# Kernel optimization log

Measured on AMD Instinct MI355X. Metric: run time of the kernel, lower is better.

Reference implementation:

```python
import jax, jax.numpy as jnp
import numpy as np

B, N_OBJ, N_REL = 32, 100, 512
D_OBJ, D_CTX, D_HID = 1024, 1024, 1024


def setup_inputs() -> dict:
    key = jax.random.key(0)
    k1, k2, k3, k4, k5 = jax.random.split(key, 5)
    object_branch_output = jax.random.normal(k1, (B * N_OBJ, D_OBJ), dtype=jnp.float32)
    context_branch_output = jax.random.normal(k2, (B, D_CTX), dtype=jnp.float32)
    num_obj = jnp.full((B,), N_OBJ, dtype=jnp.int32)
    num_rels = jnp.full((B,), N_REL, dtype=jnp.int32)
    obj_pairs = jax.random.randint(k3, (B, N_REL, 2), 0, N_OBJ, dtype=jnp.int32)
    W1 = jax.random.normal(k4, (D_OBJ + D_CTX, D_HID), dtype=jnp.float32) * (1.0 / np.sqrt(D_OBJ + D_CTX))
    b1 = jnp.zeros((D_HID,), dtype=jnp.float32)
    W2 = jax.random.normal(k5, (D_HID, D_HID), dtype=jnp.float32) * (1.0 / np.sqrt(D_HID))
    b2 = jnp.zeros((D_HID,), dtype=jnp.float32)
    return {
        "object_branch_output": object_branch_output,
        "context_branch_output": context_branch_output,
        "num_obj": num_obj,
        "num_rels": num_rels,
        "obj_pairs": obj_pairs,
        "W1": W1, "b1": b1, "W2": W2, "b2": b2,
    }


def reference(object_branch_output, context_branch_output, num_obj, num_rels,
              obj_pairs, W1, b1, W2, b2):
    # --- prepare_f_oo_vis_input, fully vectorized ---
    # per-batch object index offsets: sum(num_obj[:b])  (exclusive cumsum)
    obj_offsets = jnp.cumsum(num_obj) - num_obj                       # [B]
    global_pairs = obj_pairs + obj_offsets[:, None, None]             # [B, R, 2]
    # gather both endpoints of every pair and mean-aggregate
    pair_feats = object_branch_output[global_pairs]                   # [B, R, 2, D_obj]
    obj_vec = pair_feats.mean(axis=2)                                 # [B, R, D_obj]
    # broadcast per-batch context vector to every relation, then concat
    ctx = jnp.broadcast_to(context_branch_output[:, None, :],
                           obj_vec.shape[:2] + (context_branch_output.shape[-1],))
    input_f_oo_vis = jnp.concatenate([obj_vec, ctx], axis=-1)         # [B, R, D_obj+D_ctx]
    x = input_f_oo_vis.reshape(-1, input_f_oo_vis.shape[-1])          # [tot_rels, D_obj+D_ctx]
    # --- f_oo_vis MLP: (Linear -> ReLU) per layer pair ---
    h = jax.nn.relu(x @ W1 + b1)
    f_oo_vis_output = jax.nn.relu(h @ W2 + b2)
    return object_branch_output, f_oo_vis_output
```

## Files before the change

kernel.cpp:

```cpp
#include <hip/hip_runtime.h>
#include <hip/hip_bf16.h>

#define BB   32
#define NREL 512
#define DD   1024
#define MTOT (BB * NREL)
#define OBJ_ROWS (BB * 100)

typedef __attribute__((ext_vector_type(8))) short bf16x8;
typedef __attribute__((ext_vector_type(4))) float f32x4;

__device__ __forceinline__ unsigned short f2bf(float f) {
    union { float f; unsigned u; } v; v.f = f;
    unsigned r = v.u + 0x7fff + ((v.u >> 16) & 1);
    return (unsigned short)(r >> 16);
}

__device__ __forceinline__ float bf2f(unsigned short s) {
    union { unsigned u; float f; } v; v.u = (unsigned)s << 16;
    return v.f;
}

__device__ __forceinline__ void gld16(const void* g, void* l) {
    __builtin_amdgcn_global_load_lds(
        (const __attribute__((address_space(1))) unsigned int*)g,
        (__attribute__((address_space(3))) unsigned int*)l,
        16, 0, 0);
}

__device__ __forceinline__ void barfence() {
    asm volatile("" ::: "memory");
    __builtin_amdgcn_s_barrier();
    asm volatile("" ::: "memory");
}

__global__ void __launch_bounds__(256) prep_kernel(
    const float* __restrict__ obj, const float* __restrict__ ctx,
    const float* __restrict__ W1, const float* __restrict__ W2,
    unsigned short* __restrict__ W1t, unsigned short* __restrict__ W2t,
    float* __restrict__ part, unsigned short* __restrict__ obj_bf,
    float* __restrict__ out_obj) {
    __shared__ float smem[32 * 33];
    int bid = blockIdx.x;
    int tid = threadIdx.x;

    if (bid < 1024) {
        int slice = bid & 3, chunk = (bid >> 2) & 7, b = bid >> 5;
        int nl = tid & 127, kh = tid >> 7;
        int n = chunk * 128 + nl;
        int kbase = slice * 256 + kh * 128;
        const float* c = ctx + (size_t)b * DD + kbase;
        const float* w = W1 + (size_t)(DD + kbase) * DD + n;
        float a0 = 0.f, a1 = 0.f, a2 = 0.f, a3 = 0.f;
#pragma unroll 8
        for (int k = 0; k < 128; k += 4) {
            a0 = fmaf(c[k + 0], w[(size_t)(k + 0) * DD], a0);
            a1 = fmaf(c[k + 1], w[(size_t)(k + 1) * DD], a1);
            a2 = fmaf(c[k + 2], w[(size_t)(k + 2) * DD], a2);
            a3 = fmaf(c[k + 3], w[(size_t)(k + 3) * DD], a3);
        }
        smem[kh * 128 + nl] = (a0 + a1) + (a2 + a3);
        __syncthreads();
        if (kh == 0)
            part[(((size_t)slice * BB + b) << 10) + n] = smem[nl] + smem[128 + nl];
    } else if (bid < 3072) {
        const float* W = (bid < 2048) ? W1 : W2;
        unsigned short* Wt = (bid < 2048) ? W1t : W2t;
        int t = (bid - 1024) & 1023;
        int k0 = (t >> 5) * 32, n0 = (t & 31) * 32;
        int tr = tid >> 5, tc = tid & 31;
#pragma unroll
        for (int i = 0; i < 4; i++)
            smem[(tr + i * 8) * 33 + tc] = W[(size_t)(k0 + tr + i * 8) * DD + n0 + tc];
        __syncthreads();
#pragma unroll
        for (int i = 0; i < 4; i++)
            Wt[(size_t)(n0 + tr + i * 8) * DD + k0 + tc] = f2bf(smem[tc * 33 + tr + i * 8]);
    } else {
        const float4* src = (const float4*)obj;
        float4* dst = (float4*)out_obj;
        ushort4* dbf = (ushort4*)obj_bf;
        for (int i = (bid - 3072) * 256 + tid; i < OBJ_ROWS * DD / 4; i += 2048 * 256) {
            float4 v = src[i];
            dst[i] = v;
            ushort4 o;
            o.x = f2bf(v.x); o.y = f2bf(v.y); o.z = f2bf(v.z); o.w = f2bf(v.w);
            dbf[i] = o;
        }
    }
}

__global__ void __launch_bounds__(256) gemmP_kernel(
    const unsigned short* __restrict__ A,
    const unsigned short* __restrict__ Bt,
    unsigned short* __restrict__ P) {
    constexpr int K = 1024;
    __shared__ __attribute__((aligned(16))) unsigned short As[64 * 32];
    __shared__ __attribute__((aligned(16))) unsigned short Bs[128 * 32];
    int tid = threadIdx.x;
    int lane = tid & 63, wave = tid >> 6;
    int wr = wave >> 1, wc = wave & 1;
    int mBase = blockIdx.y * 64;
    int nBase = blockIdx.x * 128;

    f32x4 acc[2][4];
#pragma unroll
    for (int i = 0; i < 2; i++)
#pragma unroll
        for (int j = 0; j < 4; j++) acc[i][j] = (f32x4){0.f, 0.f, 0.f, 0.f};

    const unsigned short* Ab = A + (size_t)mBase * K;
    const unsigned short* Bb = Bt + (size_t)nBase * K;

    int arow = tid >> 2, akc = (tid & 3) * 8;

    for (int k0 = 0; k0 < K; k0 += 32) {
        gld16(Ab + (size_t)arow * K + k0 + akc, As + tid * 8);
#pragma unroll
        for (int hh = 0; hh < 2; hh++) {
            int c = tid + hh * 256;
            int row = c >> 2, kc = (c & 3) * 8;
            gld16(Bb + (size_t)row * K + k0 + kc, Bs + c * 8);
        }
        __syncthreads();
        int lr = lane & 15, kg = (lane >> 4) * 8;
        bf16x8 af[2], bfr[4];
#pragma unroll
        for (int m = 0; m < 2; m++)
            af[m] = *(const bf16x8*)&As[(wr * 32 + m * 16 + lr) * 32 + kg];
#pragma unroll
        for (int n = 0; n < 4; n++)
            bfr[n] = *(const bf16x8*)&Bs[(wc * 64 + n * 16 + lr) * 32 + kg];
#pragma unroll
        for (int m = 0; m < 2; m++)
#pragma unroll
            for (int n = 0; n < 4; n++)
                acc[m][n] = __builtin_amdgcn_mfma_f32_16x16x32_bf16(af[m], bfr[n], acc[m][n], 0, 0, 0);
        __syncthreads();
    }

    int lr = lane & 15, rg = (lane >> 4) * 4;
#pragma unroll
    for (int m = 0; m < 2; m++)
#pragma unroll
        for (int n = 0; n < 4; n++) {
            int col = nBase + wc * 64 + n * 16 + lr;
#pragma unroll
            for (int r = 0; r < 4; r++) {
                int row = mBase + wr * 32 + m * 16 + rg + r;
                P[(size_t)row * DD + col] = f2bf(acc[m][n][r]);
            }
        }
}

__global__ void __launch_bounds__(256) hgen_kernel(
    const unsigned short* __restrict__ P, const int* __restrict__ pairs,
    const int* __restrict__ num_obj, const float* __restrict__ part,
    const float* __restrict__ b1, unsigned short* __restrict__ h) {
    int rbase = blockIdx.x * 16;
    int b = rbase >> 9;
    int off = 0;
    for (int i = 0; i < b; i++) off += num_obj[i];
    int t = threadIdx.x;

    float4 bv = ((const float4*)b1)[t];
#pragma unroll
    for (int s = 0; s < 4; s++) {
        float4 p = ((const float4*)(part + (((size_t)s * BB + b) << 10)))[t];
        bv.x += p.x; bv.y += p.y; bv.z += p.z; bv.w += p.w;
    }

#pragma unroll 4
    for (int rr = 0; rr < 16; rr++) {
        int row = rbase + rr;
        int i0 = pairs[2 * row] + off;
        int i1 = pairs[2 * row + 1] + off;
        ushort4 a = ((const ushort4*)(P + (size_t)i0 * DD))[t];
        ushort4 c = ((const ushort4*)(P + (size_t)i1 * DD))[t];
        float v0 = 0.5f * (bf2f(a.x) + bf2f(c.x)) + bv.x;
        float v1 = 0.5f * (bf2f(a.y) + bf2f(c.y)) + bv.y;
        float v2 = 0.5f * (bf2f(a.z) + bf2f(c.z)) + bv.z;
        float v3 = 0.5f * (bf2f(a.w) + bf2f(c.w)) + bv.w;
        ushort4 o;
        o.x = f2bf(v0 > 0.f ? v0 : 0.f);
        o.y = f2bf(v1 > 0.f ? v1 : 0.f);
        o.z = f2bf(v2 > 0.f ? v2 : 0.f);
        o.w = f2bf(v3 > 0.f ? v3 : 0.f);
        ((ushort4*)(h + (size_t)row * DD))[t] = o;
    }
}

__global__ void __launch_bounds__(512, 2) gemm2_kernel(
    const unsigned short* __restrict__ A,
    const unsigned short* __restrict__ Bt,
    const float* __restrict__ bias,
    float* __restrict__ Cout) {
    constexpr int K = 1024;
    constexpr int NT = K / 64;
    extern __shared__ unsigned short lds[];
    int tid = threadIdx.x;
    int lane = tid & 63, wave = tid >> 6;
    int wr = wave >> 2, wc = wave & 3;
    int lr = lane & 15, g = lane >> 4;

    int wg = blockIdx.x;
    int swz = (wg & 7) * 32 + (wg >> 3);
    int mBase = (swz >> 2) * 256;
    int nBase = (swz & 3) * 256;

    const unsigned short* Ab = A + (size_t)mBase * K;
    const unsigned short* Bb = Bt + (size_t)nBase * K;

    int srow[4], soff[4], sdst[4];
#pragma unroll
    for (int i = 0; i < 4; i++) {
        int s = i * 512 + tid;
        int row = s >> 3, cperm = s & 7;
        srow[i] = row;
        soff[i] = (cperm ^ (row & 7)) * 8;
        sdst[i] = s * 8;
    }

    f32x4 acc[8][4];
#pragma unroll
    for (int i = 0; i < 8; i++)
#pragma unroll
        for (int j = 0; j < 4; j++) acc[i][j] = (f32x4){0.f, 0.f, 0.f, 0.f};

    auto STAGE = [&](int bi, int kt) {
        unsigned short* Ad = lds + bi * 16384;
        unsigned short* Bd = lds + 32768 + bi * 16384;
        int ko = kt * 64;
#pragma unroll
        for (int i = 0; i < 4; i++) {
            gld16(Ab + (size_t)srow[i] * K + ko + soff[i], Ad + sdst[i]);
            gld16(Bb + (size_t)srow[i] * K + ko + soff[i], Bd + sdst[i]);
        }
    };

    auto COMPUTE = [&](int bi) {
        const unsigned short* As = lds + bi * 16384;
        const unsigned short* Bs = lds + 32768 + bi * 16384;
        bf16x8 bfr[4][2];
#pragma unroll
        for (int n = 0; n < 4; n++)
#pragma unroll
            for (int kk = 0; kk < 2; kk++) {
                int row = wc * 64 + n * 16 + lr;
                int c = kk * 4 + g;
                bfr[n][kk] = *(const bf16x8*)&Bs[row * 64 + ((c ^ (row & 7)) * 8)];
            }
#pragma unroll
        for (int half = 0; half < 2; half++) {
            bf16x8 af[4][2];
#pragma unroll
            for (int m = 0; m < 4; m++)
#pragma unroll
                for (int kk = 0; kk < 2; kk++) {
                    int row = wr * 128 + (half * 4 + m) * 16 + lr;
                    int c = kk * 4 + g;
                    af[m][kk] = *(const bf16x8*)&As[row * 64 + ((c ^ (row & 7)) * 8)];
                }
            __builtin_amdgcn_s_setprio(1);
#pragma unroll
            for (int m = 0; m < 4; m++)
#pragma unroll
                for (int n = 0; n < 4; n++)
#pragma unroll
                    for (int kk = 0; kk < 2; kk++)
                        acc[half * 4 + m][n] = __builtin_amdgcn_mfma_f32_16x16x32_bf16(
                            af[m][kk], bfr[n][kk], acc[half * 4 + m][n], 0, 0, 0);
            __builtin_amdgcn_s_setprio(0);
        }
    };

    STAGE(0, 0);
    int cur = 0;
    for (int kt = 0; kt < NT - 1; ++kt) {
        STAGE(cur ^ 1, kt + 1);
        asm volatile("s_waitcnt vmcnt(8)" ::: "memory");
        barfence();
        COMPUTE(cur);
        barfence();
        cur ^= 1;
    }
    asm volatile("s_waitcnt vmcnt(0)" ::: "memory");
    barfence();
    COMPUTE(cur);

    int rg = g * 4;
#pragma unroll
    for (int m = 0; m < 8; m++) {
#pragma unroll
        for (int n = 0; n < 4; n++) {
            int col = nBase + wc * 64 + n * 16 + lr;
            float bv = bias[col];
#pragma unroll
            for (int r = 0; r < 4; r++) {
                int row = mBase + wr * 128 + m * 16 + rg + r;
                float v = acc[m][n][r] + bv;
                Cout[(size_t)row * 1024 + col] = v > 0.f ? v : 0.f;
            }
        }
    }
}

extern "C" void kernel_launch(void* const* d_in, const int* in_sizes, int n_in,
                              void* d_out, int out_size, void* d_ws, size_t ws_size,
                              hipStream_t stream) {
    (void)in_sizes; (void)n_in; (void)out_size; (void)ws_size;
    const float* obj     = (const float*)d_in[0];
    const float* ctx     = (const float*)d_in[1];
    const int*   num_obj = (const int*)d_in[2];
    const int*   pairs   = (const int*)d_in[4];
    const float* W1      = (const float*)d_in[5];
    const float* b1      = (const float*)d_in[6];
    const float* W2      = (const float*)d_in[7];
    const float* b2      = (const float*)d_in[8];

    char* ws = (char*)d_ws;
    unsigned short* obj_bf = (unsigned short*)(ws);
    unsigned short* P      = (unsigned short*)(ws + 6553600);
    unsigned short* h      = (unsigned short*)(ws + 13107200);
    unsigned short* W1t    = (unsigned short*)(ws + 46661632);
    unsigned short* W2t    = (unsigned short*)(ws + 48758784);

    float* out_obj = (float*)d_out;
    float* out_f   = out_obj + (size_t)OBJ_ROWS * DD;
    float* part    = out_f;

    hipFuncSetAttribute(reinterpret_cast<const void*>(gemm2_kernel),
                        hipFuncAttributeMaxDynamicSharedMemorySize, 131072);

    prep_kernel<<<dim3(5120), 256, 0, stream>>>(
        obj, ctx, W1, W2, W1t, W2t, part, obj_bf, out_obj);
    gemmP_kernel<<<dim3(8, 50), 256, 0, stream>>>(obj_bf, W1t, P);
    hgen_kernel<<<dim3(1024), 256, 0, stream>>>(P, pairs, num_obj, part, b1, h);
    gemm2_kernel<<<dim3(256), 512, 131072, stream>>>(h, W2t, b2, out_f);
}
```

Baseline: 91.90 us.

## Fuse pair gather-mean and bias/ReLU into second GEMM's A-tile staging

```diff
diff --git a/kernel.cpp b/kernel.cpp
--- a/kernel.cpp
+++ b/kernel.cpp
@@ -93,15 +93,32 @@
 __global__ void __launch_bounds__(256) gemmP_kernel(
     const unsigned short* __restrict__ A,
     const unsigned short* __restrict__ Bt,
-    unsigned short* __restrict__ P) {
+    unsigned short* __restrict__ P,
+    const float* __restrict__ part,
+    const float* __restrict__ b1,
+    float* __restrict__ cbias) {
     constexpr int K = 1024;
     __shared__ __attribute__((aligned(16))) unsigned short As[64 * 32];
     __shared__ __attribute__((aligned(16))) unsigned short Bs[128 * 32];
+    int bid = blockIdx.x;
     int tid = threadIdx.x;
+
+    if (bid >= 400) {
+        int b = bid - 400;
+        float4 v = ((const float4*)b1)[tid];
+#pragma unroll
+        for (int s = 0; s < 4; s++) {
+            float4 p = ((const float4*)(part + (((size_t)s * BB + b) << 10)))[tid];
+            v.x += p.x; v.y += p.y; v.z += p.z; v.w += p.w;
+        }
+        ((float4*)(cbias + ((size_t)b << 10)))[tid] = v;
+        return;
+    }
+
     int lane = tid & 63, wave = tid >> 6;
     int wr = wave >> 1, wc = wave & 1;
-    int mBase = blockIdx.y * 64;
-    int nBase = blockIdx.x * 128;
+    int mBase = (bid >> 3) * 64;
+    int nBase = (bid & 7) * 128;
 
     f32x4 acc[2][4];
 #pragma unroll
@@ -153,45 +170,11 @@
         }
 }
 
-__global__ void __launch_bounds__(256) hgen_kernel(
-    const unsigned short* __restrict__ P, const int* __restrict__ pairs,
-    const int* __restrict__ num_obj, const float* __restrict__ part,
-    const float* __restrict__ b1, unsigned short* __restrict__ h) {
-    int rbase = blockIdx.x * 16;
-    int b = rbase >> 9;
-    int off = 0;
-    for (int i = 0; i < b; i++) off += num_obj[i];
-    int t = threadIdx.x;
-
-    float4 bv = ((const float4*)b1)[t];
-#pragma unroll
-    for (int s = 0; s < 4; s++) {
-        float4 p = ((const float4*)(part + (((size_t)s * BB + b) << 10)))[t];
-        bv.x += p.x; bv.y += p.y; bv.z += p.z; bv.w += p.w;
-    }
-
-#pragma unroll 4
-    for (int rr = 0; rr < 16; rr++) {
-        int row = rbase + rr;
-        int i0 = pairs[2 * row] + off;
-        int i1 = pairs[2 * row + 1] + off;
-        ushort4 a = ((const ushort4*)(P + (size_t)i0 * DD))[t];
-        ushort4 c = ((const ushort4*)(P + (size_t)i1 * DD))[t];
-        float v0 = 0.5f * (bf2f(a.x) + bf2f(c.x)) + bv.x;
-        float v1 = 0.5f * (bf2f(a.y) + bf2f(c.y)) + bv.y;
-        float v2 = 0.5f * (bf2f(a.z) + bf2f(c.z)) + bv.z;
-        float v3 = 0.5f * (bf2f(a.w) + bf2f(c.w)) + bv.w;
-        ushort4 o;
-        o.x = f2bf(v0 > 0.f ? v0 : 0.f);
-        o.y = f2bf(v1 > 0.f ? v1 : 0.f);
-        o.z = f2bf(v2 > 0.f ? v2 : 0.f);
-        o.w = f2bf(v3 > 0.f ? v3 : 0.f);
-        ((ushort4*)(h + (size_t)row * DD))[t] = o;
-    }
-}
-
-__global__ void __launch_bounds__(512, 2) gemm2_kernel(
-    const unsigned short* __restrict__ A,
+__global__ void __launch_bounds__(512, 2) gemm2f_kernel(
+    const unsigned short* __restrict__ P,
+    const int* __restrict__ pairs,
+    const int* __restrict__ num_obj,
+    const float* __restrict__ cbias,
     const unsigned short* __restrict__ Bt,
     const float* __restrict__ bias,
     float* __restrict__ Cout) {
@@ -208,10 +191,16 @@
     int mBase = (swz >> 2) * 256;
     int nBase = (swz & 3) * 256;
 
-    const unsigned short* Ab = A + (size_t)mBase * K;
+    int b = mBase >> 9;
+    int off = 0;
+    for (int i = 0; i < b; i++) off += num_obj[i];
+    const float* cbb = cbias + ((size_t)b << 10);
+
     const unsigned short* Bb = Bt + (size_t)nBase * K;
 
     int srow[4], soff[4], sdst[4];
+    const unsigned short* pA[4];
+    const unsigned short* pB[4];
 #pragma unroll
     for (int i = 0; i < 4; i++) {
         int s = i * 512 + tid;
@@ -219,6 +208,9 @@
         srow[i] = row;
         soff[i] = (cperm ^ (row & 7)) * 8;
         sdst[i] = s * 8;
+        int grow = mBase + row;
+        pA[i] = P + (size_t)(pairs[2 * grow] + off) * DD + soff[i];
+        pB[i] = P + (size_t)(pairs[2 * grow + 1] + off) * DD + soff[i];
     }
 
     f32x4 acc[8][4];
@@ -227,14 +219,41 @@
 #pragma unroll
         for (int j = 0; j < 4; j++) acc[i][j] = (f32x4){0.f, 0.f, 0.f, 0.f};
 
-    auto STAGE = [&](int bi, int kt) {
-        unsigned short* Ad = lds + bi * 16384;
+    bf16x8 ra0[4], ra1[4];
+
+    auto BSTAGE = [&](int bi, int kt) {
         unsigned short* Bd = lds + 32768 + bi * 16384;
         int ko = kt * 64;
 #pragma unroll
+        for (int i = 0; i < 4; i++)
+            gld16(Bb + (size_t)srow[i] * K + ko + soff[i], Bd + sdst[i]);
+    };
+
+    auto ALOAD = [&](int kt) {
+#pragma unroll
         for (int i = 0; i < 4; i++) {
-            gld16(Ab + (size_t)srow[i] * K + ko + soff[i], Ad + sdst[i]);
-            gld16(Bb + (size_t)srow[i] * K + ko + soff[i], Bd + sdst[i]);
+            ra0[i] = *(const bf16x8*)(pA[i] + kt * 64);
+            ra1[i] = *(const bf16x8*)(pB[i] + kt * 64);
+        }
+    };
+
+    auto AWRITE = [&](int bi, int kt) {
+        unsigned short* Ad = lds + bi * 16384;
+#pragma unroll
+        for (int i = 0; i < 4; i++) {
+            const float* cp = cbb + kt * 64 + soff[i];
+            float4 c0 = ((const float4*)cp)[0];
+            float4 c1 = ((const float4*)cp)[1];
+            float cc[8] = {c0.x, c0.y, c0.z, c0.w, c1.x, c1.y, c1.z, c1.w};
+            bf16x8 o;
+#pragma unroll
+            for (int e = 0; e < 8; e++) {
+                float v = 0.5f * (bf2f((unsigned short)ra0[i][e]) +
+                                  bf2f((unsigned short)ra1[i][e])) + cc[e];
+                v = v > 0.f ? v : 0.f;
+                o[e] = (short)f2bf(v);
+            }
+            *(bf16x8*)(Ad + sdst[i]) = o;
         }
     };
 
@@ -274,19 +293,26 @@
         }
     };
 
-    STAGE(0, 0);
+    ALOAD(0);
+    BSTAGE(0, 0);
+    asm volatile("s_waitcnt vmcnt(0)" ::: "memory");
+    AWRITE(0, 0);
+    asm volatile("s_waitcnt lgkmcnt(0)" ::: "memory");
+    barfence();
+
     int cur = 0;
-    for (int kt = 0; kt < NT - 1; ++kt) {
-        STAGE(cur ^ 1, kt + 1);
-        asm volatile("s_waitcnt vmcnt(8)" ::: "memory");
-        barfence();
+    for (int kt = 0; kt < NT; ++kt) {
+        if (kt + 1 < NT) BSTAGE(cur ^ 1, kt + 1);
         COMPUTE(cur);
+        if (kt + 1 < NT) {
+            ALOAD(kt + 1);
+            asm volatile("s_waitcnt vmcnt(0)" ::: "memory");
+            AWRITE(cur ^ 1, kt + 1);
+        }
+        asm volatile("s_waitcnt lgkmcnt(0)" ::: "memory");
         barfence();
         cur ^= 1;
     }
-    asm volatile("s_waitcnt vmcnt(0)" ::: "memory");
-    barfence();
-    COMPUTE(cur);
 
     int rg = g * 4;
 #pragma unroll
@@ -321,7 +347,7 @@
     char* ws = (char*)d_ws;
     unsigned short* obj_bf = (unsigned short*)(ws);
     unsigned short* P      = (unsigned short*)(ws + 6553600);
-    unsigned short* h      = (unsigned short*)(ws + 13107200);
+    float*          cbias  = (float*)(ws + 13107200);
     unsigned short* W1t    = (unsigned short*)(ws + 46661632);
     unsigned short* W2t    = (unsigned short*)(ws + 48758784);
 
@@ -329,12 +355,12 @@
     float* out_f   = out_obj + (size_t)OBJ_ROWS * DD;
     float* part    = out_f;
 
-    hipFuncSetAttribute(reinterpret_cast<const void*>(gemm2_kernel),
+    hipFuncSetAttribute(reinterpret_cast<const void*>(gemm2f_kernel),
                         hipFuncAttributeMaxDynamicSharedMemorySize, 131072);
 
     prep_kernel<<<dim3(5120), 256, 0, stream>>>(
         obj, ctx, W1, W2, W1t, W2t, part, obj_bf, out_obj);
-    gemmP_kernel<<<dim3(8, 50), 256, 0, stream>>>(obj_bf, W1t, P);
-    hgen_kernel<<<dim3(1024), 256, 0, stream>>>(P, pairs, num_obj, part, b1, h);
-    gemm2_kernel<<<dim3(256), 512, 131072, stream>>>(h, W2t, b2, out_f);
-}
+    gemmP_kernel<<<dim3(432), 256, 0, stream>>>(obj_bf, W1t, P, part, b1, cbias);
+    gemm2f_kernel<<<dim3(256), 512, 131072, stream>>>(
+        P, pairs, num_obj, cbias, W2t, b2, out_f);
+}
```

New measurement: 90.39 us. About the same (-1.6%).
